# Kernel tuning notes

Measured on AMD Instinct MI355X. Metric: run time of the kernel, lower is better.

Reference implementation:

```python
import jax, jax.numpy as jnp
import numpy as np

B, N, E, D, OUT = 2, 4096, 16384, 64, 64


def setup_inputs() -> dict:
    key = jax.random.key(0)
    k_x, k_e, k_ri, k_ro, k_w1, k_b1, k_w2, k_b2 = jax.random.split(key, 8)
    X = jax.random.normal(k_x, (B, N, D), dtype=jnp.float32)
    e = jax.random.uniform(k_e, (B, E), dtype=jnp.float32)
    # 0/1 incidence matrices: each edge has exactly one in-node and one out-node
    ri_idx = jax.random.randint(k_ri, (B, E), 0, N)
    ro_idx = jax.random.randint(k_ro, (B, E), 0, N)
    Ri = jax.nn.one_hot(ri_idx, N, dtype=jnp.float32).transpose(0, 2, 1)  # [B,N,E]
    Ro = jax.nn.one_hot(ro_idx, N, dtype=jnp.float32).transpose(0, 2, 1)  # [B,N,E]
    # MLP params: Linear(3D -> OUT), Tanh, Linear(OUT -> OUT), Tanh
    lim1 = 1.0 / np.sqrt(3 * D)
    lim2 = 1.0 / np.sqrt(OUT)
    W1 = jax.random.uniform(k_w1, (3 * D, OUT), jnp.float32, -lim1, lim1)
    b1 = jax.random.uniform(k_b1, (OUT,), jnp.float32, -lim1, lim1)
    W2 = jax.random.uniform(k_w2, (OUT, OUT), jnp.float32, -lim2, lim2)
    b2 = jax.random.uniform(k_b2, (OUT,), jnp.float32, -lim2, lim2)
    return {"X": X, "e": e, "Ri": Ri, "Ro": Ro,
            "W1": W1, "b1": b1, "W2": W2, "b2": b2}


def reference(X, e, Ri, Ro, W1, b1, W2, b2):
    # gather per-edge node features: bmm(R^T, X) -> [B,E,D]
    bo = jnp.einsum('bne,bnd->bed', Ro, X)
    bi = jnp.einsum('bne,bnd->bed', Ri, X)
    # edge-weighted scatter back to nodes: bmm(R * e, .) -> [B,N,D]
    mi = jnp.einsum('bne,bed->bnd', Ri * e[:, None, :], bo)
    mo = jnp.einsum('bne,bed->bnd', Ro * e[:, None, :], bi)
    h = jnp.concatenate([mi, mo, X], axis=2)  # [B,N,3D]
    h = jnp.tanh(h @ W1 + b1)
    return jnp.tanh(h @ W2 + b2)
```

## Files before the change

kernel.cpp:

```cpp
#include <hip/hip_runtime.h>
#include <hip/hip_bf16.h>
#include <math.h>

#define BB 2
#define NN 4096
#define EE 16384
#define DD 64
#define OO 64

__global__ __launch_bounds__(256) void extract_idx_kernel(
    const float* __restrict__ Ri, const float* __restrict__ Ro,
    int* __restrict__ ri_idx, int* __restrict__ ro_idx)
{
    const unsigned total4 = (unsigned)(BB) * (unsigned)(NN) * (unsigned)(EE / 4);
    unsigned stride = gridDim.x * blockDim.x;
    for (unsigned i = blockIdx.x * blockDim.x + threadIdx.x; i < total4; i += stride) {
        float4 vi = ((const float4*)Ri)[i];
        float4 vo = ((const float4*)Ro)[i];
        unsigned fe = i * 4u;
        int e = (int)(fe & (EE - 1));
        int n = (int)((fe >> 14) & (NN - 1));
        int b = (int)(fe >> 26);
        int base = b * EE + e;
        if (vi.x != 0.f) ri_idx[base + 0] = n;
        if (vi.y != 0.f) ri_idx[base + 1] = n;
        if (vi.z != 0.f) ri_idx[base + 2] = n;
        if (vi.w != 0.f) ri_idx[base + 3] = n;
        if (vo.x != 0.f) ro_idx[base + 0] = n;
        if (vo.y != 0.f) ro_idx[base + 1] = n;
        if (vo.z != 0.f) ro_idx[base + 2] = n;
        if (vo.w != 0.f) ro_idx[base + 3] = n;
    }
}

__global__ __launch_bounds__(256) void scatter_kernel(
    const float* __restrict__ X, const float* __restrict__ ew,
    const int* __restrict__ ri_idx, const int* __restrict__ ro_idx,
    float* __restrict__ mi, float* __restrict__ mo)
{
    int t = blockIdx.x * blockDim.x + threadIdx.x;
    int edge = t >> 6;
    int lane = t & 63;
    if (edge >= BB * EE) return;
    int b = edge >> 14;
    float w = ew[edge];
    int ri = ri_idx[edge];
    int ro = ro_idx[edge];
    const float* xb = X + (size_t)b * NN * DD;
    float xro = xb[ro * DD + lane];
    float xri = xb[ri * DD + lane];
    float* mib = mi + (size_t)b * NN * DD;
    float* mob = mo + (size_t)b * NN * DD;
    atomicAdd(&mib[ri * DD + lane], w * xro);
    atomicAdd(&mob[ro * DD + lane], w * xri);
}

__global__ __launch_bounds__(64) void mlp_kernel(
    const float* __restrict__ X, const float* __restrict__ mi,
    const float* __restrict__ mo,
    const float* __restrict__ W1, const float* __restrict__ b1,
    const float* __restrict__ W2, const float* __restrict__ b2,
    float* __restrict__ out)
{
    int node = blockIdx.x * blockDim.x + threadIdx.x;
    if (node >= BB * NN) return;

    float acc[OO];
    #pragma unroll
    for (int j = 0; j < OO; ++j) acc[j] = b1[j];

    const float* srcs[3];
    srcs[0] = mi + (size_t)node * DD;
    srcs[1] = mo + (size_t)node * DD;
    srcs[2] = X  + (size_t)node * DD;

    for (int part = 0; part < 3; ++part) {
        const float* src = srcs[part];
        for (int kc = 0; kc < DD; kc += 4) {
            float4 hv = *(const float4*)(src + kc);
            const float* wrow = W1 + ((size_t)part * DD + kc) * OO;
            #pragma unroll
            for (int j = 0; j < OO; ++j) {
                acc[j] += hv.x * wrow[j]
                        + hv.y * wrow[OO + j]
                        + hv.z * wrow[2 * OO + j]
                        + hv.w * wrow[3 * OO + j];
            }
        }
    }

    #pragma unroll
    for (int j = 0; j < OO; ++j) acc[j] = tanhf(acc[j]);

    float acc2[OO];
    #pragma unroll
    for (int j = 0; j < OO; ++j) acc2[j] = b2[j];

    for (int k = 0; k < OO; ++k) {
        const float* wrow = W2 + (size_t)k * OO;
        float hk = acc[k];
        #pragma unroll
        for (int j = 0; j < OO; ++j) acc2[j] += hk * wrow[j];
    }

    float* o = out + (size_t)node * OO;
    #pragma unroll
    for (int j = 0; j < OO; ++j) o[j] = tanhf(acc2[j]);
}

extern "C" void kernel_launch(void* const* d_in, const int* in_sizes, int n_in,
                              void* d_out, int out_size, void* d_ws, size_t ws_size,
                              hipStream_t stream)
{
    const float* X  = (const float*)d_in[0];
    const float* ew = (const float*)d_in[1];
    const float* Ri = (const float*)d_in[2];
    const float* Ro = (const float*)d_in[3];
    const float* W1 = (const float*)d_in[4];
    const float* b1 = (const float*)d_in[5];
    const float* W2 = (const float*)d_in[6];
    const float* b2 = (const float*)d_in[7];
    float* out = (float*)d_out;

    float* mi = (float*)d_ws;
    float* mo = mi + (size_t)BB * NN * DD;
    int* ri_idx = (int*)(mo + (size_t)BB * NN * DD);
    int* ro_idx = ri_idx + BB * EE;

    hipMemsetAsync(mi, 0, (size_t)2 * BB * NN * DD * sizeof(float), stream);

    extract_idx_kernel<<<4096, 256, 0, stream>>>(Ri, Ro, ri_idx, ro_idx);

    scatter_kernel<<<(BB * EE * 64) / 256, 256, 0, stream>>>(
        X, ew, ri_idx, ro_idx, mi, mo);

    mlp_kernel<<<(BB * NN) / 64, 64, 0, stream>>>(
        X, mi, mo, W1, b1, W2, b2, out);
}
```

Baseline: 1.121 ms.

## Use wave-per-node MLP with shuffles and wider nontemporal loads in index extraction

The MLP kernel now gives each wavefront one node, with each lane computing one output feature and broadcasting inputs via __shfl. This replaces the old one-thread-per-node design, which held 64-element register arrays and issued uncoalesced weight reads, and it launches many more threads. The index extraction kernel now loads 8 floats per thread with nontemporal loads, tests them as integer bits instead of float compares, and halves the loop iterations. Extraction streams two 512MB matrices, so its bandwidth efficiency probably dominates total time.

```diff
diff --git a/kernel.cpp b/kernel.cpp
--- a/kernel.cpp
+++ b/kernel.cpp
@@ -8,28 +8,41 @@
 #define DD 64
 #define OO 64
 
+typedef unsigned int v4u __attribute__((ext_vector_type(4)));
+
 __global__ __launch_bounds__(256) void extract_idx_kernel(
-    const float* __restrict__ Ri, const float* __restrict__ Ro,
+    const v4u* __restrict__ Ri, const v4u* __restrict__ Ro,
     int* __restrict__ ri_idx, int* __restrict__ ro_idx)
 {
-    const unsigned total4 = (unsigned)(BB) * (unsigned)(NN) * (unsigned)(EE / 4);
+    const unsigned total8 = (unsigned)BB * NN * (EE / 8);
     unsigned stride = gridDim.x * blockDim.x;
-    for (unsigned i = blockIdx.x * blockDim.x + threadIdx.x; i < total4; i += stride) {
-        float4 vi = ((const float4*)Ri)[i];
-        float4 vo = ((const float4*)Ro)[i];
-        unsigned fe = i * 4u;
+    for (unsigned i = blockIdx.x * blockDim.x + threadIdx.x; i < total8; i += stride) {
+        unsigned i4 = i * 2u;
+        v4u a0 = __builtin_nontemporal_load(&Ri[i4]);
+        v4u a1 = __builtin_nontemporal_load(&Ri[i4 + 1]);
+        v4u c0 = __builtin_nontemporal_load(&Ro[i4]);
+        v4u c1 = __builtin_nontemporal_load(&Ro[i4 + 1]);
+        unsigned fe = i * 8u;
         int e = (int)(fe & (EE - 1));
         int n = (int)((fe >> 14) & (NN - 1));
         int b = (int)(fe >> 26);
         int base = b * EE + e;
-        if (vi.x != 0.f) ri_idx[base + 0] = n;
-        if (vi.y != 0.f) ri_idx[base + 1] = n;
-        if (vi.z != 0.f) ri_idx[base + 2] = n;
-        if (vi.w != 0.f) ri_idx[base + 3] = n;
-        if (vo.x != 0.f) ro_idx[base + 0] = n;
-        if (vo.y != 0.f) ro_idx[base + 1] = n;
-        if (vo.z != 0.f) ro_idx[base + 2] = n;
-        if (vo.w != 0.f) ro_idx[base + 3] = n;
+        if (a0.x) ri_idx[base + 0] = n;
+        if (a0.y) ri_idx[base + 1] = n;
+        if (a0.z) ri_idx[base + 2] = n;
+        if (a0.w) ri_idx[base + 3] = n;
+        if (a1.x) ri_idx[base + 4] = n;
+        if (a1.y) ri_idx[base + 5] = n;
+        if (a1.z) ri_idx[base + 6] = n;
+        if (a1.w) ri_idx[base + 7] = n;
+        if (c0.x) ro_idx[base + 0] = n;
+        if (c0.y) ro_idx[base + 1] = n;
+        if (c0.z) ro_idx[base + 2] = n;
+        if (c0.w) ro_idx[base + 3] = n;
+        if (c1.x) ro_idx[base + 4] = n;
+        if (c1.y) ro_idx[base + 5] = n;
+        if (c1.z) ro_idx[base + 6] = n;
+        if (c1.w) ro_idx[base + 7] = n;
     }
 }
 
@@ -55,57 +68,41 @@
     atomicAdd(&mob[ro * DD + lane], w * xri);
 }
 
-__global__ __launch_bounds__(64) void mlp_kernel(
+__global__ __launch_bounds__(256) void mlp_kernel(
     const float* __restrict__ X, const float* __restrict__ mi,
     const float* __restrict__ mo,
     const float* __restrict__ W1, const float* __restrict__ b1,
     const float* __restrict__ W2, const float* __restrict__ b2,
     float* __restrict__ out)
 {
-    int node = blockIdx.x * blockDim.x + threadIdx.x;
-    if (node >= BB * NN) return;
+    int wid = (blockIdx.x * blockDim.x + threadIdx.x) >> 6;
+    int lane = threadIdx.x & 63;
+    if (wid >= BB * NN) return;
 
-    float acc[OO];
-    #pragma unroll
-    for (int j = 0; j < OO; ++j) acc[j] = b1[j];
-
+    float acc = b1[lane];
     const float* srcs[3];
-    srcs[0] = mi + (size_t)node * DD;
-    srcs[1] = mo + (size_t)node * DD;
-    srcs[2] = X  + (size_t)node * DD;
+    srcs[0] = mi + (size_t)wid * DD;
+    srcs[1] = mo + (size_t)wid * DD;
+    srcs[2] = X  + (size_t)wid * DD;
 
     for (int part = 0; part < 3; ++part) {
-        const float* src = srcs[part];
-        for (int kc = 0; kc < DD; kc += 4) {
-            float4 hv = *(const float4*)(src + kc);
-            const float* wrow = W1 + ((size_t)part * DD + kc) * OO;
-            #pragma unroll
-            for (int j = 0; j < OO; ++j) {
-                acc[j] += hv.x * wrow[j]
-                        + hv.y * wrow[OO + j]
-                        + hv.z * wrow[2 * OO + j]
-                        + hv.w * wrow[3 * OO + j];
-            }
+        float fv = srcs[part][lane];
+        const float* wbase = W1 + (size_t)part * DD * OO;
+        #pragma unroll
+        for (int k = 0; k < DD; ++k) {
+            float fk = __shfl(fv, k, 64);
+            acc += fk * wbase[k * OO + lane];
         }
     }
+    float h = tanhf(acc);
 
+    float acc2 = b2[lane];
     #pragma unroll
-    for (int j = 0; j < OO; ++j) acc[j] = tanhf(acc[j]);
-
-    float acc2[OO];
-    #pragma unroll
-    for (int j = 0; j < OO; ++j) acc2[j] = b2[j];
-
     for (int k = 0; k < OO; ++k) {
-        const float* wrow = W2 + (size_t)k * OO;
-        float hk = acc[k];
-        #pragma unroll
-        for (int j = 0; j < OO; ++j) acc2[j] += hk * wrow[j];
+        float hk = __shfl(h, k, 64);
+        acc2 += hk * W2[k * OO + lane];
     }
-
-    float* o = out + (size_t)node * OO;
-    #pragma unroll
-    for (int j = 0; j < OO; ++j) o[j] = tanhf(acc2[j]);
+    out[(size_t)wid * OO + lane] = tanhf(acc2);
 }
 
 extern "C" void kernel_launch(void* const* d_in, const int* in_sizes, int n_in,
@@ -127,13 +124,14 @@
     int* ri_idx = (int*)(mo + (size_t)BB * NN * DD);
     int* ro_idx = ri_idx + BB * EE;
 
-    hipMemsetAsync(mi, 0, (size_t)2 * BB * NN * DD * sizeof(float), stream);
+    (void)hipMemsetAsync(mi, 0, (size_t)2 * BB * NN * DD * sizeof(float), stream);
 
-    extract_idx_kernel<<<4096, 256, 0, stream>>>(Ri, Ro, ri_idx, ro_idx);
+    extract_idx_kernel<<<4096, 256, 0, stream>>>(
+        (const v4u*)Ri, (const v4u*)Ro, ri_idx, ro_idx);
 
     scatter_kernel<<<(BB * EE * 64) / 256, 256, 0, stream>>>(
         X, ew, ri_idx, ro_idx, mi, mo);
 
-    mlp_kernel<<<(BB * NN) / 64, 64, 0, stream>>>(
+    mlp_kernel<<<(BB * NN * 64) / 256, 256, 0, stream>>>(
         X, mi, mo, W1, b1, W2, b2, out);
 }
```

Result: faster. 1.007 ms (-10.2%).
